# Kernel tuning notes

Hardware: AMD Instinct MI355X
Metric: run time of the kernel (lower is better)

Reference implementation:

```python
import jax, jax.numpy as jnp
import numpy as np

# LightweightConv1d config (matches init_kwargs)
C = 1024        # input_size / channels
H = 16          # num_heads
K = 7           # kernel_size (odd)
PAD = 3         # padding (same-length output)


def setup_inputs() -> dict:
    key = jax.random.key(0)
    kx, kw = jax.random.split(key)
    x = jax.random.normal(kx, (8, 4096, C), dtype=jnp.float32)   # B x T x C
    weight = jax.random.uniform(kw, (H, 1, K), dtype=jnp.float32)  # per-head kernel
    return {"x": x, "weight": weight}


def reference(x, weight):
    # x: (B, T, C); weight: (H, 1, K)
    B, T, _ = x.shape
    # weight softmax over the kernel dimension (weight_softmax=True)
    w = jax.nn.softmax(weight.reshape(H, K), axis=-1)  # (H, K)
    # weight_dropout is identity at inference (eval mode)
    # channel c uses head c % H -> tile head kernels C//H times along channel axis
    w_chan = jnp.tile(w, (C // H, 1))[:, None, :]      # (C, 1, K) depthwise kernel
    x_nct = jnp.transpose(x, (0, 2, 1))                # (B, C, T)
    y = jax.lax.conv_general_dilated(
        x_nct, w_chan,
        window_strides=(1,),
        padding=[(PAD, PAD)],
        dimension_numbers=("NCH", "OIH", "NCH"),
        feature_group_count=C,
    )                                                  # (B, C, T), same length
    return jnp.transpose(y, (0, 2, 1))                 # (B, T, C)
```

## Files before the change

### kernel.cpp

```cpp
#include <hip/hip_runtime.h>


constexpr int B_   = 8;
constexpr int T_   = 4096;
constexpr int C_   = 1024;
constexpr int H_   = 16;
constexpr int K_   = 7;
constexpr int PAD_ = 3;
constexpr int TCHUNK = 8;
constexpr int W_  = TCHUNK + K_ - 1;
constexpr int C4 = C_ / 4;

__global__ __launch_bounds__(256, 4) void lwconv_kernel(
    const float* __restrict__ x, const float* __restrict__ w,
    float* __restrict__ y) {
  __shared__ float ws[H_][K_];
  const int tid = threadIdx.x;

  if (tid < H_) {
    float v[K_];
    float m = -1e30f;
#pragma unroll
    for (int k = 0; k < K_; ++k) { v[k] = w[tid * K_ + k]; m = fmaxf(m, v[k]); }
    float s = 0.f;
#pragma unroll
    for (int k = 0; k < K_; ++k) { v[k] = expf(v[k] - m); s += v[k]; }
    const float inv = 1.f / s;
#pragma unroll
    for (int k = 0; k < K_; ++k) ws[tid][k] = v[k] * inv;
  }
  __syncthreads();

  const int h0 = (4 * tid) & (H_ - 1);
  float wr[4][K_];
#pragma unroll
  for (int j = 0; j < 4; ++j)
#pragma unroll
    for (int k = 0; k < K_; ++k) wr[j][k] = ws[h0 + j][k];

  const int nchunks = T_ / TCHUNK;
  const int b  = blockIdx.x / nchunks;
  const int t0 = (blockIdx.x % nchunks) * TCHUNK;

  const float4* __restrict__ xr =
      reinterpret_cast<const float4*>(x + (size_t)b * T_ * C_) + tid;
  float4* __restrict__ yr =
      reinterpret_cast<float4*>(y + (size_t)b * T_ * C_) + tid;

  const float4 z4 = make_float4(0.f, 0.f, 0.f, 0.f);

  float4 win[W_];
#pragma unroll
  for (int i = 0; i < W_; ++i) {
    const int t = t0 - PAD_ + i;
    win[i] = (t >= 0 && t < T_) ? xr[(size_t)t * C4] : z4;
  }

#pragma unroll
  for (int tt = 0; tt < TCHUNK; ++tt) {
    float ax = 0.f, ay = 0.f, az = 0.f, aw = 0.f;
#pragma unroll
    for (int k = 0; k < K_; ++k) {
      ax = fmaf(win[tt + k].x, wr[0][k], ax);
      ay = fmaf(win[tt + k].y, wr[1][k], ay);
      az = fmaf(win[tt + k].z, wr[2][k], az);
      aw = fmaf(win[tt + k].w, wr[3][k], aw);
    }
    yr[(size_t)(t0 + tt) * C4] = make_float4(ax, ay, az, aw);
  }
}

extern "C" void kernel_launch(void* const* d_in, const int* in_sizes, int n_in,
                              void* d_out, int out_size, void* d_ws, size_t ws_size,
                              hipStream_t stream) {
  const float* x = (const float*)d_in[0];
  const float* w = (const float*)d_in[1];
  float* y = (float*)d_out;

  const int grid = B_ * (T_ / TCHUNK);
  lwconv_kernel<<<grid, 256, 0, stream>>>(x, w, y);
}
```

Before: 232.3 us.

## Split channels across blocks, remap blocks to XCDs, use nontemporal float2 stores

Result: no change. 236.6 us (+1.9%).

```diff
diff --git a/kernel.cpp b/kernel.cpp
--- a/kernel.cpp
+++ b/kernel.cpp
@@ -9,9 +9,15 @@
 constexpr int PAD_ = 3;
 constexpr int TCHUNK = 8;
 constexpr int W_  = TCHUNK + K_ - 1;
-constexpr int C4 = C_ / 4;
+constexpr int NCHUNK = T_ / TCHUNK;
+constexpr int CSPLIT = 2;
+constexpr int CH  = C_ / CSPLIT;
+constexpr int C2  = C_ / 2;
+constexpr int NXCD = 8;
 
-__global__ __launch_bounds__(256, 4) void lwconv_kernel(
+typedef float vfloat2 __attribute__((ext_vector_type(2)));
+
+__global__ __launch_bounds__(256, 8) void lwconv_kernel(
     const float* __restrict__ x, const float* __restrict__ w,
     float* __restrict__ y) {
   __shared__ float ws[H_][K_];
@@ -31,42 +37,46 @@
   }
   __syncthreads();
 
-  const int h0 = (4 * tid) & (H_ - 1);
-  float wr[4][K_];
+  const int cpx = (B_ * CSPLIT * NCHUNK) / NXCD;
+  const int wid = ((int)blockIdx.x % NXCD) * cpx + (int)blockIdx.x / NXCD;
+  const int pair  = wid / NCHUNK;
+  const int tc    = wid % NCHUNK;
+  const int b     = pair & (B_ - 1);
+  const int chalf = pair >> 3;
+  const int t0    = tc * TCHUNK;
+
+  const int h0 = (2 * tid) & (H_ - 1);
+  float wr[2][K_];
 #pragma unroll
-  for (int j = 0; j < 4; ++j)
+  for (int j = 0; j < 2; ++j)
 #pragma unroll
     for (int k = 0; k < K_; ++k) wr[j][k] = ws[h0 + j][k];
 
-  const int nchunks = T_ / TCHUNK;
-  const int b  = blockIdx.x / nchunks;
-  const int t0 = (blockIdx.x % nchunks) * TCHUNK;
+  const float2* __restrict__ xr =
+      reinterpret_cast<const float2*>(x + (size_t)b * T_ * C_ + chalf * CH) + tid;
+  vfloat2* __restrict__ yr =
+      reinterpret_cast<vfloat2*>(y + (size_t)b * T_ * C_ + chalf * CH) + tid;
 
-  const float4* __restrict__ xr =
-      reinterpret_cast<const float4*>(x + (size_t)b * T_ * C_) + tid;
-  float4* __restrict__ yr =
-      reinterpret_cast<float4*>(y + (size_t)b * T_ * C_) + tid;
+  const float2 z2 = make_float2(0.f, 0.f);
 
-  const float4 z4 = make_float4(0.f, 0.f, 0.f, 0.f);
-
-  float4 win[W_];
+  float2 win[W_];
 #pragma unroll
   for (int i = 0; i < W_; ++i) {
     const int t = t0 - PAD_ + i;
-    win[i] = (t >= 0 && t < T_) ? xr[(size_t)t * C4] : z4;
+    win[i] = (t >= 0 && t < T_) ? xr[(size_t)t * C2] : z2;
   }
 
 #pragma unroll
   for (int tt = 0; tt < TCHUNK; ++tt) {
-    float ax = 0.f, ay = 0.f, az = 0.f, aw = 0.f;
+    float ax = 0.f, ay = 0.f;
 #pragma unroll
     for (int k = 0; k < K_; ++k) {
       ax = fmaf(win[tt + k].x, wr[0][k], ax);
       ay = fmaf(win[tt + k].y, wr[1][k], ay);
-      az = fmaf(win[tt + k].z, wr[2][k], az);
-      aw = fmaf(win[tt + k].w, wr[3][k], aw);
     }
-    yr[(size_t)(t0 + tt) * C4] = make_float4(ax, ay, az, aw);
+    vfloat2 out;
+    out.x = ax; out.y = ay;
+    __builtin_nontemporal_store(out, yr + (size_t)(t0 + tt) * C2);
   }
 }
 
@@ -77,6 +87,6 @@
   const float* w = (const float*)d_in[1];
   float* y = (float*)d_out;
 
-  const int grid = B_ * (T_ / TCHUNK);
+  const int grid = B_ * CSPLIT * NCHUNK;
   lwconv_kernel<<<grid, 256, 0, stream>>>(x, w, y);
 }
```
